# Performance work log

Measured on AMD Instinct MI355X. Metric: run time of the kernel, lower is better.

Reference implementation:

```python
import jax, jax.numpy as jnp
import numpy as np

N, K, P = 40000, 32, 15
C = 128            # output_feature_dim (kpconv in/out channels)
H_POS, D_POS = 64, 256
H_AGG, D_PROC = 256, 256
RADIUS = 1.0
KP_EXTENT = RADIUS / (P ** (1.0 / 3.0) - 1.0) * 1.5
SLOPE = 0.01       # nn.LeakyReLU default
EPS = 1e-5         # BatchNorm1d default eps


def _lin(key, din, dout):
    k1, k2 = jax.random.split(key)
    lim = 1.0 / np.sqrt(din)
    w = jax.random.uniform(k1, (din, dout), minval=-lim, maxval=lim, dtype=jnp.float32)
    b = jax.random.uniform(k2, (dout,), minval=-lim, maxval=lim, dtype=jnp.float32)
    return w, b


def _bn(x, g, b):
    # BatchNorm1d in training mode: biased batch statistics
    m = jnp.mean(x, axis=0)
    v = jnp.var(x, axis=0)
    return (x - m) * jax.lax.rsqrt(v + EPS) * g + b


def _lrelu(x):
    return jnp.where(x >= 0, x, SLOPE * x)


def setup_inputs() -> dict:
    key = jax.random.key(0)
    ks = jax.random.split(key, 16)
    inp = {}
    inp['points'] = jax.random.normal(ks[0], (N, 3), dtype=jnp.float32) * 10.0
    inp['covariances'] = jax.random.normal(ks[1], (N, 9), dtype=jnp.float32)
    inp['neighbors_index'] = jax.random.randint(ks[2], (N, K), 0, N)
    inp['pre_w'], inp['pre_b'] = _lin(ks[3], 9, C)
    inp['pre_bn_g'] = jnp.ones((C,), jnp.float32); inp['pre_bn_b'] = jnp.zeros((C,), jnp.float32)
    kp = jax.random.normal(ks[4], (P, 3), dtype=jnp.float32)
    kp = kp / jnp.linalg.norm(kp, axis=1, keepdims=True)
    inp['kernel_points'] = kp * jax.random.uniform(ks[5], (P, 1), dtype=jnp.float32) * RADIUS
    inp['kp_weights'] = jax.random.normal(ks[6], (P, C, C), dtype=jnp.float32) * (1.0 / np.sqrt(P * C))
    inp['pos_w1'], inp['pos_b1'] = _lin(ks[7], 3, H_POS)
    inp['pos_bn1_g'] = jnp.ones((H_POS,), jnp.float32); inp['pos_bn1_b'] = jnp.zeros((H_POS,), jnp.float32)
    inp['pos_w2'], inp['pos_b2'] = _lin(ks[8], H_POS, D_POS)
    inp['pos_bn2_g'] = jnp.ones((D_POS,), jnp.float32); inp['pos_bn2_b'] = jnp.zeros((D_POS,), jnp.float32)
    inp['agg_w1'], inp['agg_b1'] = _lin(ks[9], C, H_AGG)
    inp['agg_bn1_g'] = jnp.ones((H_AGG,), jnp.float32); inp['agg_bn1_b'] = jnp.zeros((H_AGG,), jnp.float32)
    inp['agg_w2'], inp['agg_b2'] = _lin(ks[10], H_AGG, D_PROC)
    inp['agg_bn2_g'] = jnp.ones((D_PROC,), jnp.float32); inp['agg_bn2_b'] = jnp.zeros((D_PROC,), jnp.float32)
    inp['keep_w1'], inp['keep_b1'] = _lin(ks[11], D_PROC, D_PROC // 4)
    inp['keep_bn_g'] = jnp.ones((D_PROC // 4,), jnp.float32); inp['keep_bn_b'] = jnp.zeros((D_PROC // 4,), jnp.float32)
    inp['keep_w2'], inp['keep_b2'] = _lin(ks[12], D_PROC // 4, 1)
    du = D_PROC + D_POS
    inp['uniq_w1'], inp['uniq_b1'] = _lin(ks[13], du, du // 4)
    inp['uniq_bn_g'] = jnp.ones((du // 4,), jnp.float32); inp['uniq_bn_b'] = jnp.zeros((du // 4,), jnp.float32)
    inp['uniq_w2'], inp['uniq_b2'] = _lin(ks[14], du // 4, 1)
    return inp


def reference(points, covariances, neighbors_index,
              pre_w, pre_b, pre_bn_g, pre_bn_b,
              kernel_points, kp_weights,
              pos_w1, pos_b1, pos_bn1_g, pos_bn1_b,
              pos_w2, pos_b2, pos_bn2_g, pos_bn2_b,
              agg_w1, agg_b1, agg_bn1_g, agg_bn1_b,
              agg_w2, agg_b2, agg_bn2_g, agg_bn2_b,
              keep_w1, keep_b1, keep_bn_g, keep_bn_b, keep_w2, keep_b2,
              uniq_w1, uniq_b1, uniq_bn_g, uniq_bn_b, uniq_w2, uniq_b2):
    # preactivation on 9-dim flattened covariances
    features = _lrelu(_bn(covariances @ pre_w + pre_b, pre_bn_g, pre_bn_b))  # [N, C]

    # ---- rigid KPConv (linear influence, sum aggregation, shadow point at index N) ----
    s_pad = jnp.concatenate([points, jnp.full((1, 3), 1e6, points.dtype)], axis=0)
    x_pad = jnp.concatenate([features, jnp.zeros((1, C), features.dtype)], axis=0)
    nb = s_pad[neighbors_index] - points[:, None, :]                          # [N, K, 3]
    # squared distances to kernel points without materializing [N,K,P,3]
    sq = (jnp.sum(nb * nb, -1)[:, :, None]
          + jnp.sum(kernel_points * kernel_points, -1)[None, None, :]
          - 2.0 * jnp.einsum('nkd,pd->nkp', nb, kernel_points))               # [N, K, P]
    infl = jnp.maximum(1.0 - jnp.sqrt(jnp.maximum(sq, 0.0)) / KP_EXTENT, 0.0)  # [N, K, P]
    nx = x_pad[neighbors_index]                                               # [N, K, C]
    weighted = jnp.einsum('nkp,nkc->npc', infl, nx)                           # [N, P, C]
    conv = jnp.einsum('npc,pcd->nd', weighted, kp_weights)                    # [N, C]
    # density normalization: count non-shadow neighbors
    nnum = jnp.maximum(jnp.sum(jnp.sum(nx, -1) > 0.0, axis=-1), 1)
    kpconv_feature = conv / nnum[:, None].astype(conv.dtype)

    # position embedding MLP
    pos = _lrelu(_bn(points @ pos_w1 + pos_b1, pos_bn1_g, pos_bn1_b))
    pos = _lrelu(_bn(pos @ pos_w2 + pos_b2, pos_bn2_g, pos_bn2_b))            # [N, 256]

    # feature aggregation MLP
    agg = _lrelu(_bn(kpconv_feature @ agg_w1 + agg_b1, agg_bn1_g, agg_bn1_b))
    agg = _lrelu(_bn(agg @ agg_w2 + agg_b2, agg_bn2_g, agg_bn2_b))            # [N, 256]

    # heads
    kh = _lrelu(_bn(agg @ keep_w1 + keep_b1, keep_bn_g, keep_bn_b))
    match_score = jax.nn.sigmoid((kh @ keep_w2 + keep_b2).ravel())
    u_in = jnp.concatenate([pos, agg], axis=1)                                # [N, 512]
    uh = _lrelu(_bn(u_in @ uniq_w1 + uniq_b1, uniq_bn_g, uniq_bn_b))
    unique_score = jax.nn.sigmoid((uh @ uniq_w2 + uniq_b2).ravel())
    return match_score, unique_score, neighbors_index
```

## Files before the change

### kernel.cpp

```cpp
#include <hip/hip_runtime.h>
#include <math.h>


#define NPTS 40000
#define KNB  32
#define PKP  15
#define SLOPE 0.01f
#define BNEPS 1e-5f
#define INV_N (1.0f/40000.0f)

typedef __attribute__((ext_vector_type(8))) short bf16x8;
typedef __attribute__((ext_vector_type(4))) float f32x4;

__device__ __forceinline__ float lrelu(float x){ return x >= 0.0f ? x : SLOPE*x; }
__device__ __forceinline__ unsigned short f2bf(float f){
  unsigned int b = __float_as_uint(f);
  b += 0x7fffu + ((b>>16)&1u);
  return (unsigned short)(b>>16);
}
__device__ __forceinline__ float bf2f(unsigned short u){
  return __uint_as_float(((unsigned int)u)<<16);
}

__global__ __launch_bounds__(256) void k_wprep_all(
    const float* __restrict__ kpw,  const float* __restrict__ pw2,
    const float* __restrict__ aw1,  const float* __restrict__ aw2,
    const float* __restrict__ kw1,  const float* __restrict__ uw1,
    unsigned short* __restrict__ wT){
  int i = blockIdx.x*256 + threadIdx.x;
  const float* src; int K, N, off, li;
  if      (i < 245760){ src=kpw; K=1920; N=128; off=0;      li=i; }
  else if (i < 262144){ src=pw2; K=64;   N=256; off=245760; li=i-245760; }
  else if (i < 294912){ src=aw1; K=128;  N=256; off=262144; li=i-262144; }
  else if (i < 360448){ src=aw2; K=256;  N=256; off=294912; li=i-294912; }
  else if (i < 376832){ src=kw1; K=256;  N=64;  off=360448; li=i-360448; }
  else                { src=uw1; K=512;  N=128; off=376832; li=i-376832; }
  int k = li / N, n = li - k*N;
  wT[(size_t)off + (size_t)n*K + k] = f2bf(src[li]);
}

__global__ __launch_bounds__(256) void k_pre(
    const float* __restrict__ cov, const float* __restrict__ w,
    const float* __restrict__ b, unsigned short* __restrict__ preact,
    float* __restrict__ stats){
  __shared__ float sW[9*128];
  __shared__ float sX[32*9];
  __shared__ float sSum[2][128], sSq[2][128];
  int tid = threadIdx.x;
  int row0 = blockIdx.x*32;
  for (int i = tid; i < 9*128; i += 256) sW[i] = w[i];
  for (int i = tid; i < 32*9;  i += 256) sX[i] = cov[row0*9 + i];
  __syncthreads();
  int c = tid & 127, h = tid >> 7;
  float bias = b[c];
  float ls = 0.0f, lq = 0.0f;
  for (int r = h*16; r < h*16+16; ++r){
    float acc = bias;
    #pragma unroll
    for (int i = 0; i < 9; ++i) acc += sX[r*9+i]*sW[i*128+c];
    preact[(size_t)(row0+r)*128 + c] = f2bf(acc);
    ls += acc; lq += acc*acc;
  }
  sSum[h][c] = ls; sSq[h][c] = lq;
  __syncthreads();
  if (h == 0){
    atomicAdd(&stats[c],     sSum[0][c]+sSum[1][c]);
    atomicAdd(&stats[128+c], sSq[0][c]+sSq[1][c]);
  }
}

__global__ __launch_bounds__(256) void k_prenorm(
    const unsigned short* __restrict__ preact, const float* __restrict__ stats,
    const float* __restrict__ g, const float* __restrict__ b,
    unsigned short* __restrict__ feat, float* __restrict__ fsum){
  int wid  = (int)((blockIdx.x*256 + threadIdx.x) >> 6);
  int lane = threadIdx.x & 63;
  if (wid >= NPTS) return;
  float su = stats[lane], sq = stats[128+lane];
  float mean = su*INV_N, var = sq*INV_N - mean*mean;
  float s0 = g[lane]*rsqrtf(var+BNEPS), h0 = b[lane]-mean*s0;
  su = stats[64+lane]; sq = stats[192+lane];
  mean = su*INV_N; var = sq*INV_N - mean*mean;
  float s1 = g[64+lane]*rsqrtf(var+BNEPS), h1 = b[64+lane]-mean*s1;
  size_t off = (size_t)wid*128;
  float f0 = lrelu(bf2f(preact[off+lane])*s0+h0);
  float f1 = lrelu(bf2f(preact[off+64+lane])*s1+h1);
  feat[off+lane]    = f2bf(f0);
  feat[off+64+lane] = f2bf(f1);
  float t = f0 + f1;
  #pragma unroll
  for (int o = 32; o; o >>= 1) t += __shfl_down(t, o, 64);
  if (lane == 0) fsum[wid] = t;
}

__global__ __launch_bounds__(256) void k_scan(
    const float* __restrict__ pts, const int* __restrict__ nbr,
    const float* __restrict__ kp, const float* __restrict__ fsum,
    float* __restrict__ invn, int* __restrict__ list,
    int* __restrict__ gcount, float ext2){
  __shared__ float sKP[45];
  if (threadIdx.x < 45) sKP[threadIdx.x] = kp[threadIdx.x];
  __syncthreads();
  int wv   = (blockIdx.x*256 + threadIdx.x) >> 6;
  int lane = threadIdx.x & 63;
  int half = lane >> 5;
  int kk   = lane & 31;
  int n    = wv*2 + half;
  float px = pts[n*3+0], py = pts[n*3+1], pz = pts[n*3+2];
  int j = nbr[(size_t)n*KNB + kk];
  float nx = pts[j*3+0] - px;
  float ny = pts[j*3+1] - py;
  float nz = pts[j*3+2] - pz;
  float fs = fsum[j];
  bool anyp = false;
  #pragma unroll
  for (int p = 0; p < PKP; ++p){
    float dx = nx - sKP[p*3+0], dy = ny - sKP[p*3+1], dz = nz - sKP[p*3+2];
    anyp |= (dx*dx + dy*dy + dz*dz < ext2);
  }
  unsigned long long act  = __ballot(anyp);
  unsigned long long good = __ballot(fs > 0.0f);
  unsigned int actH  = half ? (unsigned int)(act  >> 32) : (unsigned int)act;
  unsigned int goodH = half ? (unsigned int)(good >> 32) : (unsigned int)good;
  if (kk == 0){
    int cnt = __popc(goodH);
    invn[n] = 1.0f / (float)(cnt < 1 ? 1 : cnt);
    if (actH){
      int pos = atomicAdd(gcount, 1);
      list[pos] = n;
    }
  }
}

__global__ __launch_bounds__(256) void k_conv_act(
    const float* __restrict__ pts, const int* __restrict__ nbr,
    const float* __restrict__ kp, const unsigned short* __restrict__ feat,
    const unsigned short* __restrict__ kpwT, const float* __restrict__ invn,
    const int* __restrict__ list, const int* __restrict__ gcount,
    unsigned short* __restrict__ kpfc, float ext2, float inv_ext){
  __shared__ float sW[PKP*128];
  __shared__ float sInfl[KNB*16];
  __shared__ unsigned int sPairP[KNB];
  __shared__ float sKP[45];
  __shared__ float sOut[128];
  __shared__ unsigned int sPmask, sPact;
  int tid = threadIdx.x;
  if (tid < 45) sKP[tid] = kp[tid];
  int cnt = *gcount;
  for (int it = blockIdx.x; it < cnt; it += gridDim.x){
    int n = list[it];
    if (tid == 0){ sPmask = 0u; sPact = 0u; }
    for (int i = tid; i < PKP*128; i += 256) sW[i] = 0.0f;
    __syncthreads();
    if (tid < KNB){
      int j = nbr[(size_t)n*KNB + tid];
      float nx = pts[j*3+0] - pts[n*3+0];
      float ny = pts[j*3+1] - pts[n*3+1];
      float nz = pts[j*3+2] - pts[n*3+2];
      unsigned int pm = 0u;
      #pragma unroll
      for (int p = 0; p < PKP; ++p){
        float dx = nx - sKP[p*3+0], dy = ny - sKP[p*3+1], dz = nz - sKP[p*3+2];
        float d2 = dx*dx + dy*dy + dz*dz;
        float infl = 0.0f;
        if (d2 < ext2){ infl = 1.0f - sqrtf(d2)*inv_ext; pm |= (1u << p); }
        sInfl[tid*16 + p] = infl;
      }
      sPairP[tid] = pm;
      if (pm){
        atomicOr(&sPact, 1u << tid);
        atomicOr(&sPmask, pm);
      }
    }
    __syncthreads();
    if (tid < 128){
      int c = tid;
      unsigned int m = sPact;
      while (m){
        int k = __ffs(m) - 1; m &= m - 1;
        int j = nbr[(size_t)n*KNB + k];
        float f = bf2f(feat[(size_t)j*128 + c]);
        unsigned int pp = sPairP[k];
        while (pp){
          int p = __ffs(pp) - 1; pp &= pp - 1;
          sW[p*128 + c] += sInfl[k*16 + p] * f;
        }
      }
    }
    __syncthreads();
    int d = tid & 127, h = tid >> 7;
    float acc = 0.0f;
    unsigned int pm = sPmask;
    while (pm){
      int p = __ffs(pm) - 1; pm &= pm - 1;
      const unsigned short* wp = kpwT + (size_t)d*1920 + p*128 + h*64;
      const float* wsrc = &sW[p*128 + h*64];
      #pragma unroll
      for (int c8 = 0; c8 < 8; ++c8){
        uint4 v = *(const uint4*)(wp + c8*8);
        unsigned int e[4] = {v.x, v.y, v.z, v.w};
        #pragma unroll
        for (int q = 0; q < 4; ++q){
          acc += wsrc[c8*8 + 2*q]     * bf2f((unsigned short)(e[q] & 0xffff));
          acc += wsrc[c8*8 + 2*q + 1] * bf2f((unsigned short)(e[q] >> 16));
        }
      }
    }
    if (h == 0) sOut[d] = acc;
    __syncthreads();
    if (h == 1) kpfc[(size_t)it*128 + d] = f2bf((sOut[d] + acc) * invn[n]);
    __syncthreads();
  }
}

__global__ __launch_bounds__(256) void k_rowgemm(
    const unsigned short* __restrict__ X, int xCompact,
    const float* __restrict__ st, const float* __restrict__ g,
    const float* __restrict__ bb, int K, int norm,
    const unsigned short* __restrict__ Wt, const float* __restrict__ bias,
    int NOUT, unsigned short* __restrict__ Y, int yCompact,
    float* __restrict__ statsOut,
    const int* __restrict__ list, const int* __restrict__ gcount){
  __shared__ float xs[256];
  __shared__ float sSc[256], sSh[256];
  int tid = threadIdx.x;
  if (norm && tid < K){
    float s = st[tid], q = st[K+tid];
    float mean = s*INV_N, var = q*INV_N - mean*mean;
    float sc = g[tid]*rsqrtf(var+BNEPS);
    sSc[tid] = sc; sSh[tid] = bb[tid] - mean*sc;
  }
  __syncthreads();
  int cnt = *gcount;
  float rs = 0.0f, rq = 0.0f;
  for (int it = blockIdx.x; it < cnt; it += gridDim.x){
    int n = list[it];
    int xi = xCompact ? it : n;
    if (tid < K){
      float xv = bf2f(X[(size_t)xi*K + tid]);
      if (norm) xv = lrelu(xv*sSc[tid] + sSh[tid]);
      xs[tid] = xv;
    }
    __syncthreads();
    if (tid < NOUT){
      float acc = bias[tid];
      const unsigned short* wp = Wt + (size_t)tid*K;
      for (int k8 = 0; k8 < K; k8 += 8){
        uint4 v = *(const uint4*)(wp + k8);
        unsigned int e[4] = {v.x, v.y, v.z, v.w};
        #pragma unroll
        for (int q = 0; q < 4; ++q){
          acc += xs[k8+2*q]   * bf2f((unsigned short)(e[q] & 0xffff));
          acc += xs[k8+2*q+1] * bf2f((unsigned short)(e[q] >> 16));
        }
      }
      int yi = yCompact ? it : n;
      Y[(size_t)yi*NOUT + tid] = f2bf(acc);
      rs += acc; rq += acc*acc;
    }
    __syncthreads();
  }
  if (tid < NOUT && rs != 0.0f){
    atomicAdd(&statsOut[tid],      rs);
    atomicAdd(&statsOut[NOUT+tid], rq);
  }
}

__global__ __launch_bounds__(256) void k_const(
    const float* __restrict__ vin, float* __restrict__ statsX, int K,
    const float* __restrict__ g, const float* __restrict__ bb,
    const unsigned short* __restrict__ Wt, const float* __restrict__ bias,
    int NOUT, float* __restrict__ vout, unsigned int* __restrict__ voutU,
    const int* __restrict__ gcount){
  __shared__ float sX[256];
  __shared__ float sV[256];
  int tid = threadIdx.x;
  float fN = (float)(NPTS - *gcount);
  if (tid < K){
    float s = vin[tid];
    statsX[tid]   += fN*s;
    statsX[K+tid] += fN*s*s;
  }
  __syncthreads();
  if (NOUT > 0){
    if (tid < K){
      float s = statsX[tid], q = statsX[K+tid];
      float mean = s*INV_N, var = q*INV_N - mean*mean;
      float sc = g[tid]*rsqrtf(var+BNEPS);
      sX[tid] = lrelu(vin[tid]*sc + bb[tid] - mean*sc);
    }
    __syncthreads();
    if (tid < NOUT){
      float acc = bias[tid];
      const unsigned short* wp = Wt + (size_t)tid*K;
      for (int k8 = 0; k8 < K; k8 += 8){
        uint4 v = *(const uint4*)(wp + k8);
        unsigned int e[4] = {v.x, v.y, v.z, v.w};
        #pragma unroll
        for (int q = 0; q < 4; ++q){
          acc += sX[k8+2*q]   * bf2f((unsigned short)(e[q] & 0xffff));
          acc += sX[k8+2*q+1] * bf2f((unsigned short)(e[q] >> 16));
        }
      }
      vout[tid] = acc; sV[tid] = acc;
    }
    __syncthreads();
    if (tid < NOUT/2)
      voutU[tid] = (unsigned int)f2bf(sV[2*tid]) |
                   ((unsigned int)f2bf(sV[2*tid+1]) << 16);
  }
}

__global__ __launch_bounds__(256) void k_fill(
    unsigned int* __restrict__ Y, const unsigned int* __restrict__ vU,
    int shift, int total){
  int i = blockIdx.x*256 + threadIdx.x;
  int stride = gridDim.x*256;
  unsigned int msk = (1u << shift) - 1u;
  for (; i < total; i += stride) Y[i] = vU[i & msk];
}

template<int NCF>
__global__ __launch_bounds__(256) void k_gemmw(
    const unsigned short* __restrict__ X0, const float* __restrict__ st0,
    const float* __restrict__ g0, const float* __restrict__ b0,
    int K0, int norm0,
    const unsigned short* __restrict__ X1, const float* __restrict__ st1,
    const float* __restrict__ g1, const float* __restrict__ b1, int K1,
    const unsigned short* __restrict__ Wt, const float* __restrict__ bias,
    unsigned short* __restrict__ Y, float* __restrict__ statsOut){
  const int NOUT = NCF*16;
  __shared__ unsigned short sA[64*64];
  __shared__ unsigned short sB[NOUT*64];
  __shared__ float sSc[64], sSh[64];
  __shared__ float sSum[NOUT], sSq[NOUT];
  int tid = threadIdx.x;
  int row0 = blockIdx.x*64;
  int w = tid >> 6, l = tid & 63;
  int KT = K0 + K1;
  if (tid < NOUT){ sSum[tid] = 0.0f; sSq[tid] = 0.0f; }
  f32x4 acc[NCF] = {};
  for (int kc = 0; kc < KT; kc += 64){
    bool sel1 = (kc >= K0);
    const unsigned short* Xp = sel1 ? X1 : X0;
    int Ks = sel1 ? K1 : K0;
    int cb = sel1 ? kc - K0 : kc;
    int nf = sel1 ? 1 : norm0;
    if (tid < 64 && nf){
      const float* st = sel1 ? st1 : st0;
      const float* gg = sel1 ? g1 : g0;
      const float* bb = sel1 ? b1 : b0;
      int ch = cb + tid;
      float s = st[ch], q = st[Ks+ch];
      float mean = s*INV_N, var = q*INV_N - mean*mean;
      float sc = gg[ch]*rsqrtf(var+BNEPS);
      sSc[tid] = sc; sSh[tid] = bb[ch] - mean*sc;
    }
    __syncthreads();
    #pragma unroll
    for (int p = 0; p < 2; ++p){
      int r = (tid >> 3) + p*32;
      int k0 = (tid & 7)*8;
      uint4 v = *(const uint4*)(Xp + (size_t)(row0+r)*Ks + cb + k0);
      if (nf){
        unsigned short e[8] = {(unsigned short)(v.x&0xffff),(unsigned short)(v.x>>16),
                               (unsigned short)(v.y&0xffff),(unsigned short)(v.y>>16),
                               (unsigned short)(v.z&0xffff),(unsigned short)(v.z>>16),
                               (unsigned short)(v.w&0xffff),(unsigned short)(v.w>>16)};
        unsigned short o[8];
        #pragma unroll
        for (int j = 0; j < 8; ++j)
          o[j] = f2bf(lrelu(bf2f(e[j])*sSc[k0+j] + sSh[k0+j]));
        v.x = (uint)o[0] | ((uint)o[1]<<16);
        v.y = (uint)o[2] | ((uint)o[3]<<16);
        v.z = (uint)o[4] | ((uint)o[5]<<16);
        v.w = (uint)o[6] | ((uint)o[7]<<16);
      }
      int byteA = (r*128 + k0*2) ^ ((r&7)<<4);
      *(uint4*)((char*)sA + byteA) = v;
    }
    #pragma unroll
    for (int ps = 0; ps < NCF/2; ++ps){
      int idx = ps*256 + tid;
      int r = idx >> 3, s = idx & 7;
      uint4 vb = *(const uint4*)(Wt + (size_t)r*KT + kc + s*8);
      int byteB = (r*128 + s*16) ^ ((r&7)<<4);
      *(uint4*)((char*)sB + byteB) = vb;
    }
    __syncthreads();
    int rowA = w*16 + (l & 15);
    #pragma unroll
    for (int m = 0; m < 2; ++m){
      int ka = m*32 + (l >> 4)*8;
      int byteA = (rowA*128 + ka*2) ^ ((rowA&7)<<4);
      bf16x8 af = *(const bf16x8*)((const char*)sA + byteA);
      #pragma unroll
      for (int cf = 0; cf < NCF; ++cf){
        int colB = cf*16 + (l & 15);
        int byteB = (colB*128 + ka*2) ^ ((colB&7)<<4);
        bf16x8 bfr = *(const bf16x8*)((const char*)sB + byteB);
        acc[cf] = __builtin_amdgcn_mfma_f32_16x16x32_bf16(af, bfr, acc[cf], 0, 0, 0);
      }
    }
    __syncthreads();
  }
  float cs[NCF], cq[NCF];
  #pragma unroll
  for (int cf = 0; cf < NCF; ++cf){
    int col = cf*16 + (l & 15);
    float bj = bias[col];
    cs[cf] = 0.0f; cq[cf] = 0.0f;
    #pragma unroll
    for (int r = 0; r < 4; ++r){
      int grow = row0 + w*16 + (l >> 4)*4 + r;
      float v = acc[cf][r] + bj;
      Y[(size_t)grow*NOUT + col] = f2bf(v);
      cs[cf] += v; cq[cf] += v*v;
    }
  }
  #pragma unroll
  for (int cf = 0; cf < NCF; ++cf){
    atomicAdd(&sSum[cf*16 + (l&15)], cs[cf]);
    atomicAdd(&sSq[cf*16 + (l&15)],  cq[cf]);
  }
  __syncthreads();
  if (tid < NOUT){
    atomicAdd(&statsOut[tid],      sSum[tid]);
    atomicAdd(&statsOut[NOUT+tid], sSq[tid]);
  }
}

__global__ __launch_bounds__(256) void k_pos1(
    const float* __restrict__ pts, const float* __restrict__ w,
    const float* __restrict__ b, unsigned short* __restrict__ p1,
    float* __restrict__ stats){
  __shared__ float sSum[4][64], sSq[4][64];
  int tid = threadIdx.x;
  int c = tid & 63, grp = tid >> 6;
  int row0 = blockIdx.x*32;
  float w0 = w[c], w1 = w[64+c], w2 = w[128+c], bb = b[c];
  float ls = 0.0f, lq = 0.0f;
  for (int r = row0 + grp*8; r < row0 + grp*8 + 8; ++r){
    float x0 = pts[r*3+0], x1 = pts[r*3+1], x2 = pts[r*3+2];
    float y = bb + x0*w0 + x1*w1 + x2*w2;
    p1[(size_t)r*64 + c] = f2bf(y);
    ls += y; lq += y*y;
  }
  sSum[grp][c] = ls; sSq[grp][c] = lq;
  __syncthreads();
  if (grp == 0){
    atomicAdd(&stats[c],    sSum[0][c]+sSum[1][c]+sSum[2][c]+sSum[3][c]);
    atomicAdd(&stats[64+c], sSq[0][c]+sSq[1][c]+sSq[2][c]+sSq[3][c]);
  }
}

__global__ __launch_bounds__(256) void k_head(
    const unsigned short* __restrict__ H, const float* __restrict__ stats,
    const float* __restrict__ g, const float* __restrict__ b,
    const float* __restrict__ w2, const float* __restrict__ b2,
    float* __restrict__ out, int Cdim){
  int wid  = (int)((blockIdx.x*256 + threadIdx.x) >> 6);
  int lane = threadIdx.x & 63;
  if (wid >= NPTS) return;
  float acc = 0.0f;
  for (int c = lane; c < Cdim; c += 64){
    float su = stats[c], sq = stats[Cdim+c];
    float mean = su*INV_N, var = sq*INV_N - mean*mean;
    float sc = g[c]*rsqrtf(var+BNEPS), sh = b[c]-mean*sc;
    float h = lrelu(bf2f(H[(size_t)wid*Cdim + c])*sc + sh);
    acc += h * w2[c];
  }
  #pragma unroll
  for (int o = 32; o; o >>= 1) acc += __shfl_down(acc, o, 64);
  if (lane == 0){
    float x = acc + b2[0];
    out[wid] = 1.0f/(1.0f + expf(-x));
  }
}

__global__ __launch_bounds__(256) void k_idx(
    const int* __restrict__ nbr, float* __restrict__ o){
  int i = blockIdx.x*256 + threadIdx.x;
  int4 v = ((const int4*)nbr)[i];
  ((float4*)o)[i] = make_float4((float)v.x,(float)v.y,(float)v.z,(float)v.w);
}

extern "C" void kernel_launch(void* const* d_in, const int* in_sizes, int n_in,
                              void* d_out, int out_size, void* d_ws, size_t ws_size,
                              hipStream_t stream) {
  const float* pts    = (const float*)d_in[0];
  const float* cov    = (const float*)d_in[1];
  const int*   nbr    = (const int*)  d_in[2];
  const float* pre_w  = (const float*)d_in[3];
  const float* pre_b  = (const float*)d_in[4];
  const float* pre_g  = (const float*)d_in[5];
  const float* pre_bb = (const float*)d_in[6];
  const float* kp     = (const float*)d_in[7];
  const float* kpw    = (const float*)d_in[8];
  const float* pos_w1 = (const float*)d_in[9];
  const float* pos_b1 = (const float*)d_in[10];
  const float* pos_g1 = (const float*)d_in[11];
  const float* pos_bb1= (const float*)d_in[12];
  const float* pos_w2 = (const float*)d_in[13];
  const float* pos_b2 = (const float*)d_in[14];
  const float* pos_g2 = (const float*)d_in[15];
  const float* pos_bb2= (const float*)d_in[16];
  const float* agg_w1 = (const float*)d_in[17];
  const float* agg_b1 = (const float*)d_in[18];
  const float* agg_g1 = (const float*)d_in[19];
  const float* agg_bb1= (const float*)d_in[20];
  const float* agg_w2 = (const float*)d_in[21];
  const float* agg_b2 = (const float*)d_in[22];
  const float* agg_g2 = (const float*)d_in[23];
  const float* agg_bb2= (const float*)d_in[24];
  const float* keep_w1= (const float*)d_in[25];
  const float* keep_b1= (const float*)d_in[26];
  const float* keep_g = (const float*)d_in[27];
  const float* keep_bb= (const float*)d_in[28];
  const float* keep_w2= (const float*)d_in[29];
  const float* keep_b2= (const float*)d_in[30];
  const float* uniq_w1= (const float*)d_in[31];
  const float* uniq_b1= (const float*)d_in[32];
  const float* uniq_g = (const float*)d_in[33];
  const float* uniq_bb= (const float*)d_in[34];
  const float* uniq_w2= (const float*)d_in[35];
  const float* uniq_b2= (const float*)d_in[36];

  float* out = (float*)d_out;

  char* wsb = (char*)d_ws;
  size_t off = 0;
  float* stats = (float*)(wsb + off); off += 4096*4;
  int*   gcount = (int*)(stats + 2304);
  float* v2  = stats + 2560;
  unsigned int* v2u = (unsigned int*)(stats + 2816);
  float* v3  = stats + 2944;
  unsigned int* v3u = (unsigned int*)(stats + 3008);
  unsigned short* wT = (unsigned short*)(wsb + off); off += (size_t)442368*2;
  unsigned short* kpwT   = wT;
  unsigned short* posw2T = wT + 245760;
  unsigned short* aggw1T = wT + 262144;
  unsigned short* aggw2T = wT + 294912;
  unsigned short* keepw1T= wT + 360448;
  unsigned short* uniqw1T= wT + 376832;
  float* fsum  = (float*)(wsb + off); off += (size_t)NPTS*4;
  float* invn  = (float*)(wsb + off); off += (size_t)NPTS*4;
  int*   list  = (int*)  (wsb + off); off += (size_t)NPTS*4;
  unsigned short* feat = (unsigned short*)(wsb + off); off += (size_t)NPTS*128*2;
  unsigned short* kpfc = (unsigned short*)(wsb + off); off += (size_t)NPTS*128*2;
  unsigned short* a1c  = (unsigned short*)(wsb + off); off += (size_t)NPTS*256*2;
  unsigned short* a2   = (unsigned short*)(wsb + off); off += (size_t)NPTS*256*2;
  unsigned short* k1   = (unsigned short*)(wsb + off); off += (size_t)NPTS*64*2;
  unsigned short* preact = a2;
  unsigned short* p1 = feat;
  unsigned short* p2 = a1c;
  unsigned short* u1 = kpfc;

  const double kpe = 1.0 / (cbrt(15.0) - 1.0) * 1.5;
  const float inv_ext = (float)(1.0 / kpe);
  const float ext2 = (float)(kpe * kpe);

  hipMemsetAsync(stats, 0, 2308*sizeof(float), stream);

  k_wprep_all<<<1728, 256, 0, stream>>>(kpw, pos_w2, agg_w1, agg_w2,
                                        keep_w1, uniq_w1, wT);

  k_pre<<<1250, 256, 0, stream>>>(cov, pre_w, pre_b, preact, stats + 0);
  k_prenorm<<<10000, 256, 0, stream>>>(preact, stats + 0, pre_g, pre_bb, feat, fsum);

  k_scan<<<5000, 256, 0, stream>>>(pts, nbr, kp, fsum, invn, list, gcount, ext2);
  k_conv_act<<<1024, 256, 0, stream>>>(pts, nbr, kp, feat, kpwT, invn,
                                       list, gcount, kpfc, ext2, inv_ext);

  k_pos1<<<1250, 256, 0, stream>>>(pts, pos_w1, pos_b1, p1, stats + 256);

  k_rowgemm<<<256, 256, 0, stream>>>(
      kpfc, 1, nullptr, nullptr, nullptr, 128, 0,
      aggw1T, agg_b1, 256, a1c, 1, stats + 896, list, gcount);
  k_const<<<1, 256, 0, stream>>>(
      agg_b1, stats + 896, 256, agg_g1, agg_bb1,
      aggw2T, agg_b2, 256, v2, v2u, gcount);
  k_fill<<<2048, 256, 0, stream>>>((unsigned int*)a2, v2u, 7, NPTS*128);
  k_rowgemm<<<256, 256, 0, stream>>>(
      a1c, 1, stats + 896, agg_g1, agg_bb1, 256, 1,
      aggw2T, agg_b2, 256, a2, 0, stats + 1408, list, gcount);
  k_const<<<1, 256, 0, stream>>>(
      v2, stats + 1408, 256, agg_g2, agg_bb2,
      keepw1T, keep_b1, 64, v3, v3u, gcount);
  k_fill<<<2048, 256, 0, stream>>>((unsigned int*)k1, v3u, 5, NPTS*32);
  k_rowgemm<<<256, 256, 0, stream>>>(
      a2, 0, stats + 1408, agg_g2, agg_bb2, 256, 1,
      keepw1T, keep_b1, 64, k1, 0, stats + 1920, list, gcount);
  k_const<<<1, 256, 0, stream>>>(
      v3, stats + 1920, 64, nullptr, nullptr,
      nullptr, nullptr, 0, nullptr, nullptr, gcount);

  k_gemmw<16><<<625, 256, 0, stream>>>(
      p1, stats + 256, pos_g1, pos_bb1, 64, 1,
      nullptr, nullptr, nullptr, nullptr, 0,
      posw2T, pos_b2, p2, stats + 384);

  k_head<<<10000, 256, 0, stream>>>(k1, stats + 1920, keep_g, keep_bb,
                                    keep_w2, keep_b2, out, 64);

  k_gemmw<8><<<625, 256, 0, stream>>>(
      p2, stats + 384, pos_g2, pos_bb2, 256, 1,
      a2, stats + 1408, agg_g2, agg_bb2, 256,
      uniqw1T, uniq_b1, u1, stats + 2048);
  k_head<<<10000, 256, 0, stream>>>(u1, stats + 2048, uniq_g, uniq_bb,
                                    uniq_w2, uniq_b2, out + NPTS, 128);

  k_idx<<<1250, 256, 0, stream>>>(nbr, out + 2*NPTS);
}
```

Measured before the change: 314.7 us.

## Compute BN stats analytically from moments and exploit sparse active rows end-to-end

Replaces the pre-layer GEMM-then-normalize passes with input moment accumulation, so BatchNorm statistics for the pre and first position layers are derived in closed form. The feature and position MLP stages are fused into single kernels. The aggregation chain now stays compact over active rows: a constant row value is propagated for inactive points instead of filling full buffers. The uniqueness GEMM is split into a dense position part with an effective bias plus a sparse delta for active rows. This removes large intermediate writes and fill kernels, at the cost of variance computed from raw moments, which may lose precision.

```diff
diff --git a/kernel.cpp b/kernel.cpp
--- a/kernel.cpp
+++ b/kernel.cpp
@@ -21,6 +21,7 @@
 __device__ __forceinline__ float bf2f(unsigned short u){
   return __uint_as_float(((unsigned int)u)<<16);
 }
+
 
 __global__ __launch_bounds__(256) void k_wprep_all(
     const float* __restrict__ kpw,  const float* __restrict__ pw2,
@@ -39,58 +40,104 @@
   wT[(size_t)off + (size_t)n*K + k] = f2bf(src[li]);
 }
 
-__global__ __launch_bounds__(256) void k_pre(
-    const float* __restrict__ cov, const float* __restrict__ w,
-    const float* __restrict__ b, unsigned short* __restrict__ preact,
+__global__ __launch_bounds__(256) void k_moments(
+    const float* __restrict__ cov, const float* __restrict__ pts,
+    float* __restrict__ mom){
+  int tid = threadIdx.x;
+  int lane = tid & 63;
+  int wv = (blockIdx.x*256 + tid) >> 6;
+  int nw = gridDim.x*4;
+  int kind = -1, ia = 0, ib = 0;
+  if (lane < 9){ kind = 0; ia = lane; }
+  else if (lane < 54){ int t = lane-9; int i = 0; while (t >= 9-i){ t -= 9-i; ++i; } kind = 1; ia = i; ib = i+t; }
+  else if (lane < 57){ kind = 2; ia = lane-54; }
+  else if (lane < 63){ int t = lane-57; int i = 0; while (t >= 3-i){ t -= 3-i; ++i; } kind = 3; ia = i; ib = i+t; }
+  float part = 0.0f;
+  for (int n = wv; n < NPTS; n += nw){
+    float v = 0.0f;
+    if (kind == 0) v = cov[n*9+ia];
+    else if (kind == 1) v = cov[n*9+ia]*cov[n*9+ib];
+    else if (kind == 2) v = pts[n*3+ia];
+    else if (kind == 3) v = pts[n*3+ia]*pts[n*3+ib];
+    part += v;
+  }
+  if (kind >= 0) atomicAdd(&mom[lane], part);
+}
+
+__global__ __launch_bounds__(256) void k_bnsetup(
+    const float* __restrict__ preW, const float* __restrict__ preB,
+    const float* __restrict__ preG, const float* __restrict__ preBB,
+    const float* __restrict__ posW1, const float* __restrict__ posB1,
+    const float* __restrict__ posG1, const float* __restrict__ posBB1,
     float* __restrict__ stats){
-  __shared__ float sW[9*128];
-  __shared__ float sX[32*9];
-  __shared__ float sSum[2][128], sSq[2][128];
-  int tid = threadIdx.x;
-  int row0 = blockIdx.x*32;
-  for (int i = tid; i < 9*128; i += 256) sW[i] = w[i];
-  for (int i = tid; i < 32*9;  i += 256) sX[i] = cov[row0*9 + i];
-  __syncthreads();
-  int c = tid & 127, h = tid >> 7;
-  float bias = b[c];
-  float ls = 0.0f, lq = 0.0f;
-  for (int r = h*16; r < h*16+16; ++r){
-    float acc = bias;
-    #pragma unroll
-    for (int i = 0; i < 9; ++i) acc += sX[r*9+i]*sW[i*128+c];
-    preact[(size_t)(row0+r)*128 + c] = f2bf(acc);
-    ls += acc; lq += acc*acc;
-  }
-  sSum[h][c] = ls; sSq[h][c] = lq;
-  __syncthreads();
-  if (h == 0){
-    atomicAdd(&stats[c],     sSum[0][c]+sSum[1][c]);
-    atomicAdd(&stats[128+c], sSq[0][c]+sSq[1][c]);
-  }
-}
-
-__global__ __launch_bounds__(256) void k_prenorm(
-    const unsigned short* __restrict__ preact, const float* __restrict__ stats,
-    const float* __restrict__ g, const float* __restrict__ b,
-    unsigned short* __restrict__ feat, float* __restrict__ fsum){
-  int wid  = (int)((blockIdx.x*256 + threadIdx.x) >> 6);
-  int lane = threadIdx.x & 63;
-  if (wid >= NPTS) return;
-  float su = stats[lane], sq = stats[128+lane];
-  float mean = su*INV_N, var = sq*INV_N - mean*mean;
-  float s0 = g[lane]*rsqrtf(var+BNEPS), h0 = b[lane]-mean*s0;
-  su = stats[64+lane]; sq = stats[192+lane];
-  mean = su*INV_N; var = sq*INV_N - mean*mean;
-  float s1 = g[64+lane]*rsqrtf(var+BNEPS), h1 = b[64+lane]-mean*s1;
-  size_t off = (size_t)wid*128;
-  float f0 = lrelu(bf2f(preact[off+lane])*s0+h0);
-  float f1 = lrelu(bf2f(preact[off+64+lane])*s1+h1);
-  feat[off+lane]    = f2bf(f0);
-  feat[off+64+lane] = f2bf(f1);
-  float t = f0 + f1;
-  #pragma unroll
-  for (int o = 32; o; o >>= 1) t += __shfl_down(t, o, 64);
-  if (lane == 0) fsum[wid] = t;
+  int tid = threadIdx.x;
+  const float* mom = stats + 2320;
+  if (tid < 128){
+    int c = tid;
+    float wv[9];
+    #pragma unroll
+    for (int i = 0; i < 9; ++i) wv[i] = preW[i*128+c];
+    float b = preB[c];
+    float mw = 0.0f;
+    #pragma unroll
+    for (int i = 0; i < 9; ++i) mw += wv[i]*mom[i];
+    mw *= INV_N;
+    float quad = 0.0f;
+    for (int i = 0; i < 9; ++i)
+      for (int j = 0; j < 9; ++j){
+        int ii = i < j ? i : j, jj = i < j ? j : i;
+        quad += wv[i]*wv[j]*mom[9 + ii*9 - (ii*(ii-1))/2 + (jj-ii)];
+      }
+    quad *= INV_N;
+    float mean = mw + b;
+    float var = quad + 2.0f*b*mw + b*b - mean*mean;
+    float sc = preG[c]*rsqrtf(var+BNEPS);
+    stats[c]     = sc;
+    stats[128+c] = preBB[c] - mean*sc + sc*b;
+  } else if (tid < 192){
+    int c = tid - 128;
+    float w0 = posW1[c], w1 = posW1[64+c], w2 = posW1[128+c];
+    float b = posB1[c];
+    const float* pm = mom + 54;
+    const float* pM = mom + 57;
+    float mw = (w0*pm[0] + w1*pm[1] + w2*pm[2])*INV_N;
+    float quad = (w0*w0*pM[0] + w1*w1*pM[3] + w2*w2*pM[5]
+               + 2.0f*(w0*w1*pM[1] + w0*w2*pM[2] + w1*w2*pM[4]))*INV_N;
+    float mean = mw + b;
+    float var = quad + 2.0f*b*mw + b*b - mean*mean;
+    float sc = posG1[c]*rsqrtf(var+BNEPS);
+    stats[256+c] = sc;
+    stats[320+c] = posBB1[c] - mean*sc + sc*b;
+  }
+}
+
+__global__ __launch_bounds__(256) void k_feat(
+    const float* __restrict__ cov, const float* __restrict__ preW,
+    const float* __restrict__ stats, unsigned short* __restrict__ feat,
+    float* __restrict__ fsum){
+  __shared__ float sW[1152];
+  __shared__ float sRed[4];
+  int tid = threadIdx.x;
+  for (int i = tid; i < 1152; i += 256) sW[i] = preW[i];
+  int c = tid & 127, g = tid >> 7;
+  float sc = stats[c], sh = stats[128+c];
+  __syncthreads();
+  for (int base = blockIdx.x*2; base < NPTS; base += gridDim.x*2){
+    int row = base + g;
+    float pre = 0.0f;
+    #pragma unroll
+    for (int i = 0; i < 9; ++i) pre += cov[row*9+i]*sW[i*128+c];
+    float f = lrelu(sc*pre + sh);
+    feat[(size_t)row*128 + c] = f2bf(f);
+    float t = f;
+    #pragma unroll
+    for (int o = 32; o; o >>= 1) t += __shfl_down(t, o, 64);
+    if ((tid & 63) == 0) sRed[tid>>6] = t;
+    __syncthreads();
+    if (tid == 0)   fsum[base]   = sRed[0] + sRed[1];
+    if (tid == 128) fsum[base+1] = sRed[2] + sRed[3];
+    __syncthreads();
+  }
 }
 
 __global__ __launch_bounds__(256) void k_scan(
@@ -213,13 +260,71 @@
   }
 }
 
+__global__ __launch_bounds__(256) void k_pos(
+    const float* __restrict__ pts, const float* __restrict__ posW1,
+    const float* __restrict__ stats, const unsigned short* __restrict__ w2T,
+    const float* __restrict__ b2, unsigned short* __restrict__ p2,
+    float* __restrict__ st384){
+  __shared__ unsigned short sW[16384];
+  __shared__ float sX[4][64];
+  __shared__ unsigned short sP2[1024];
+  int tid = threadIdx.x;
+  #pragma unroll
+  for (int ps = 0; ps < 8; ++ps){
+    int idx = ps*256 + tid;
+    int r = idx >> 3, s = idx & 7;
+    uint4 v = *(const uint4*)(w2T + (size_t)r*64 + s*8);
+    *(uint4*)((char*)sW + ((r*128 + s*16) ^ ((r&7)<<4))) = v;
+  }
+  int k = tid & 63, g = tid >> 6;
+  float w0 = posW1[k], w1 = posW1[64+k], w2 = posW1[128+k];
+  float sc1 = stats[256+k], sh1 = stats[320+k];
+  int c = tid;
+  float b2c = b2[c];
+  float cs = 0.0f, cq = 0.0f;
+  __syncthreads();
+  for (int base = blockIdx.x*4; base < NPTS; base += gridDim.x*4){
+    int row = base + g;
+    float x0 = pts[row*3+0], x1 = pts[row*3+1], x2 = pts[row*3+2];
+    sX[g][k] = lrelu(sc1*(x0*w0 + x1*w1 + x2*w2) + sh1);
+    __syncthreads();
+    float acc[4] = {b2c, b2c, b2c, b2c};
+    #pragma unroll
+    for (int k8 = 0; k8 < 64; k8 += 8){
+      uint4 v = *(const uint4*)((const char*)sW + ((c*128 + k8*2) ^ ((c&7)<<4)));
+      unsigned int e[4] = {v.x, v.y, v.z, v.w};
+      #pragma unroll
+      for (int q = 0; q < 4; ++q){
+        float wlo = bf2f((unsigned short)(e[q] & 0xffff));
+        float whi = bf2f((unsigned short)(e[q] >> 16));
+        #pragma unroll
+        for (int r = 0; r < 4; ++r)
+          acc[r] += sX[r][k8+2*q]*wlo + sX[r][k8+2*q+1]*whi;
+      }
+    }
+    #pragma unroll
+    for (int r = 0; r < 4; ++r){
+      cs += acc[r]; cq += acc[r]*acc[r];
+      sP2[r*256 + c] = f2bf(acc[r]);
+    }
+    __syncthreads();
+    if (tid < 128){
+      int r = tid >> 5, c8 = tid & 31;
+      uint4 v = *(const uint4*)(sP2 + r*256 + c8*8);
+      *(uint4*)(p2 + (size_t)(base+r)*256 + c8*8) = v;
+    }
+    __syncthreads();
+  }
+  atomicAdd(&st384[c], cs);
+  atomicAdd(&st384[256+c], cq);
+}
+
 __global__ __launch_bounds__(256) void k_rowgemm(
-    const unsigned short* __restrict__ X, int xCompact,
+    const unsigned short* __restrict__ X,
     const float* __restrict__ st, const float* __restrict__ g,
     const float* __restrict__ bb, int K, int norm,
     const unsigned short* __restrict__ Wt, const float* __restrict__ bias,
-    int NOUT, unsigned short* __restrict__ Y, int yCompact,
-    float* __restrict__ statsOut,
+    int NOUT, unsigned short* __restrict__ Y, float* __restrict__ statsOut,
     const int* __restrict__ list, const int* __restrict__ gcount){
   __shared__ float xs[256];
   __shared__ float sSc[256], sSh[256];
@@ -234,10 +339,8 @@
   int cnt = *gcount;
   float rs = 0.0f, rq = 0.0f;
   for (int it = blockIdx.x; it < cnt; it += gridDim.x){
-    int n = list[it];
-    int xi = xCompact ? it : n;
     if (tid < K){
-      float xv = bf2f(X[(size_t)xi*K + tid]);
+      float xv = bf2f(X[(size_t)it*K + tid]);
       if (norm) xv = lrelu(xv*sSc[tid] + sSh[tid]);
       xs[tid] = xv;
     }
@@ -254,8 +357,7 @@
           acc += xs[k8+2*q+1] * bf2f((unsigned short)(e[q] >> 16));
         }
       }
-      int yi = yCompact ? it : n;
-      Y[(size_t)yi*NOUT + tid] = f2bf(acc);
+      Y[(size_t)it*NOUT + tid] = f2bf(acc);
       rs += acc; rq += acc*acc;
     }
     __syncthreads();
@@ -266,34 +368,256 @@
   }
 }
 
-__global__ __launch_bounds__(256) void k_const(
-    const float* __restrict__ vin, float* __restrict__ statsX, int K,
+__global__ __launch_bounds__(256) void k_const1(
+    const float* __restrict__ b1, const float* __restrict__ g1,
+    const float* __restrict__ bb1, const unsigned short* __restrict__ aggw2T,
+    const float* __restrict__ b2, float* __restrict__ st896,
+    float* __restrict__ v2, const int* __restrict__ gcount){
+  __shared__ float sX[256];
+  int tid = threadIdx.x;
+  float fN = (float)(NPTS - *gcount);
+  float s = b1[tid];
+  st896[tid]     += fN*s;
+  st896[256+tid] += fN*s*s;
+  float su = st896[tid], sq = st896[256+tid];
+  float mean = su*INV_N, var = sq*INV_N - mean*mean;
+  float sc = g1[tid]*rsqrtf(var+BNEPS);
+  sX[tid] = lrelu(s*sc + bb1[tid] - mean*sc);
+  __syncthreads();
+  float acc = b2[tid];
+  const unsigned short* wp = aggw2T + (size_t)tid*256;
+  for (int k8 = 0; k8 < 256; k8 += 8){
+    uint4 v = *(const uint4*)(wp + k8);
+    unsigned int e[4] = {v.x, v.y, v.z, v.w};
+    #pragma unroll
+    for (int q = 0; q < 4; ++q){
+      acc += sX[k8+2*q]   * bf2f((unsigned short)(e[q] & 0xffff));
+      acc += sX[k8+2*q+1] * bf2f((unsigned short)(e[q] >> 16));
+    }
+  }
+  v2[tid] = acc;
+}
+
+__global__ __launch_bounds__(256) void k_const2(
+    const float* __restrict__ v2, const float* __restrict__ g2,
+    const float* __restrict__ bb2, const unsigned short* __restrict__ keepw1T,
+    const float* __restrict__ kb1, const unsigned short* __restrict__ uw1T,
+    const float* __restrict__ ub1, float* __restrict__ st1408,
+    float* __restrict__ v3, float* __restrict__ ub_eff,
+    const int* __restrict__ gcount){
+  __shared__ float sX[256];
+  int tid = threadIdx.x;
+  float fN = (float)(NPTS - *gcount);
+  float s = v2[tid];
+  st1408[tid]     += fN*s;
+  st1408[256+tid] += fN*s*s;
+  float su = st1408[tid], sq = st1408[256+tid];
+  float mean = su*INV_N, var = sq*INV_N - mean*mean;
+  float sc = g2[tid]*rsqrtf(var+BNEPS);
+  sX[tid] = lrelu(s*sc + bb2[tid] - mean*sc);
+  __syncthreads();
+  if (tid < 64){
+    float acc = kb1[tid];
+    const unsigned short* wp = keepw1T + (size_t)tid*256;
+    for (int k8 = 0; k8 < 256; k8 += 8){
+      uint4 v = *(const uint4*)(wp + k8);
+      unsigned int e[4] = {v.x, v.y, v.z, v.w};
+      #pragma unroll
+      for (int q = 0; q < 4; ++q){
+        acc += sX[k8+2*q]   * bf2f((unsigned short)(e[q] & 0xffff));
+        acc += sX[k8+2*q+1] * bf2f((unsigned short)(e[q] >> 16));
+      }
+    }
+    v3[tid] = acc;
+  } else if (tid < 192){
+    int c = tid - 64;
+    float acc = ub1[c];
+    const unsigned short* wp = uw1T + (size_t)c*512 + 256;
+    for (int k8 = 0; k8 < 256; k8 += 8){
+      uint4 v = *(const uint4*)(wp + k8);
+      unsigned int e[4] = {v.x, v.y, v.z, v.w};
+      #pragma unroll
+      for (int q = 0; q < 4; ++q){
+        acc += sX[k8+2*q]   * bf2f((unsigned short)(e[q] & 0xffff));
+        acc += sX[k8+2*q+1] * bf2f((unsigned short)(e[q] >> 16));
+      }
+    }
+    ub_eff[c] = acc;
+  }
+}
+
+__global__ __launch_bounds__(64) void k_const3(
+    const float* __restrict__ v3, const float* __restrict__ g3,
+    const float* __restrict__ bb3, const float* __restrict__ kw2,
+    const float* __restrict__ kb2, float* __restrict__ st1920,
+    float* __restrict__ s3out, const int* __restrict__ gcount){
+  int tid = threadIdx.x;
+  float fN = (float)(NPTS - *gcount);
+  float s = v3[tid];
+  st1920[tid]    += fN*s;
+  st1920[64+tid] += fN*s*s;
+  float su = st1920[tid], sq = st1920[64+tid];
+  float mean = su*INV_N, var = sq*INV_N - mean*mean;
+  float sc = g3[tid]*rsqrtf(var+BNEPS);
+  float h = lrelu(s*sc + bb3[tid] - mean*sc) * kw2[tid];
+  #pragma unroll
+  for (int o = 32; o; o >>= 1) h += __shfl_down(h, o, 64);
+  if (tid == 0) s3out[0] = 1.0f/(1.0f + expf(-(h + kb2[0])));
+}
+
+__global__ __launch_bounds__(256) void k_out(
+    const int* __restrict__ nbr, const float* __restrict__ s3p,
+    float* __restrict__ out){
+  int i = blockIdx.x*256 + threadIdx.x;
+  if (i < NPTS) out[i] = s3p[0];
+  int4 v = ((const int4*)nbr)[i];
+  ((float4*)(out + 2*NPTS))[i] =
+      make_float4((float)v.x,(float)v.y,(float)v.z,(float)v.w);
+}
+
+__global__ __launch_bounds__(256) void k_keepact(
+    const unsigned short* __restrict__ k1c, const float* __restrict__ st1920,
+    const float* __restrict__ g3, const float* __restrict__ b3,
+    const float* __restrict__ w2, const float* __restrict__ b2,
+    float* __restrict__ out, const int* __restrict__ list,
+    const int* __restrict__ gcount){
+  int tid = threadIdx.x;
+  int lane = tid & 63;
+  int wv = (blockIdx.x*256 + tid) >> 6;
+  int nw = gridDim.x*4;
+  float su = st1920[lane], sq = st1920[64+lane];
+  float mean = su*INV_N, var = sq*INV_N - mean*mean;
+  float sc = g3[lane]*rsqrtf(var+BNEPS);
+  float sh = b3[lane] - mean*sc;
+  float w2v = w2[lane];
+  int cnt = *gcount;
+  for (int it = wv; it < cnt; it += nw){
+    float h = lrelu(bf2f(k1c[(size_t)it*64 + lane])*sc + sh) * w2v;
+    #pragma unroll
+    for (int o = 32; o; o >>= 1) h += __shfl_down(h, o, 64);
+    if (lane == 0) out[list[it]] = 1.0f/(1.0f + expf(-(h + b2[0])));
+  }
+}
+
+__global__ __launch_bounds__(256) void k_ugemm(
+    const unsigned short* __restrict__ X, const float* __restrict__ st,
     const float* __restrict__ g, const float* __restrict__ bb,
     const unsigned short* __restrict__ Wt, const float* __restrict__ bias,
-    int NOUT, float* __restrict__ vout, unsigned int* __restrict__ voutU,
+    unsigned short* __restrict__ Y, float* __restrict__ statsOut){
+  __shared__ unsigned short sA[4096];
+  __shared__ unsigned short sB[8704];
+  __shared__ float sSc[64], sSh[64];
+  __shared__ float sSum[128], sSq[128];
+  int tid = threadIdx.x;
+  int row0 = blockIdx.x*64;
+  int w = tid >> 6, l = tid & 63;
+  if (tid < 128){ sSum[tid] = 0.0f; sSq[tid] = 0.0f; }
+  f32x4 acc[8] = {};
+  for (int kc = 0; kc < 256; kc += 64){
+    if (tid < 64){
+      int ch = kc + tid;
+      float s = st[ch], q = st[256+ch];
+      float mean = s*INV_N, var = q*INV_N - mean*mean;
+      float sc = g[ch]*rsqrtf(var+BNEPS);
+      sSc[tid] = sc; sSh[tid] = bb[ch] - mean*sc;
+    }
+    __syncthreads();
+    #pragma unroll
+    for (int p = 0; p < 2; ++p){
+      int r = (tid >> 3) + p*32;
+      int k0 = (tid & 7)*8;
+      uint4 v = *(const uint4*)(X + (size_t)(row0+r)*256 + kc + k0);
+      unsigned short e[8] = {(unsigned short)(v.x&0xffff),(unsigned short)(v.x>>16),
+                             (unsigned short)(v.y&0xffff),(unsigned short)(v.y>>16),
+                             (unsigned short)(v.z&0xffff),(unsigned short)(v.z>>16),
+                             (unsigned short)(v.w&0xffff),(unsigned short)(v.w>>16)};
+      unsigned short o[8];
+      #pragma unroll
+      for (int j = 0; j < 8; ++j)
+        o[j] = f2bf(lrelu(bf2f(e[j])*sSc[k0+j] + sSh[k0+j]));
+      v.x = (uint)o[0] | ((uint)o[1]<<16);
+      v.y = (uint)o[2] | ((uint)o[3]<<16);
+      v.z = (uint)o[4] | ((uint)o[5]<<16);
+      v.w = (uint)o[6] | ((uint)o[7]<<16);
+      *(uint4*)((char*)sA + ((r*128 + k0*2) ^ ((r&7)<<4))) = v;
+    }
+    #pragma unroll
+    for (int ps = 0; ps < 4; ++ps){
+      int idx = ps*256 + tid;
+      int r = idx >> 3, s = idx & 7;
+      uint4 vb = *(const uint4*)(Wt + (size_t)r*512 + kc + s*8);
+      *(uint4*)((char*)sB + ((r*128 + s*16) ^ ((r&7)<<4))) = vb;
+    }
+    __syncthreads();
+    int rowA = w*16 + (l & 15);
+    #pragma unroll
+    for (int m = 0; m < 2; ++m){
+      int ka = m*32 + (l >> 4)*8;
+      bf16x8 af = *(const bf16x8*)((const char*)sA + ((rowA*128 + ka*2) ^ ((rowA&7)<<4)));
+      #pragma unroll
+      for (int cf = 0; cf < 8; ++cf){
+        int colB = cf*16 + (l & 15);
+        bf16x8 bfr = *(const bf16x8*)((const char*)sB + ((colB*128 + ka*2) ^ ((colB&7)<<4)));
+        acc[cf] = __builtin_amdgcn_mfma_f32_16x16x32_bf16(af, bfr, acc[cf], 0, 0, 0);
+      }
+    }
+    __syncthreads();
+  }
+  #pragma unroll
+  for (int cf = 0; cf < 8; ++cf){
+    int col = cf*16 + (l & 15);
+    float bj = bias[col];
+    float cs = 0.0f, cq = 0.0f;
+    #pragma unroll
+    for (int r = 0; r < 4; ++r){
+      int rr = w*16 + (l >> 4)*4 + r;
+      float v = acc[cf][r] + bj;
+      sB[rr*136 + col] = f2bf(v);
+      cs += v; cq += v*v;
+    }
+    atomicAdd(&sSum[col], cs);
+    atomicAdd(&sSq[col],  cq);
+  }
+  __syncthreads();
+  #pragma unroll
+  for (int ps = 0; ps < 4; ++ps){
+    int idx = ps*256 + tid;
+    int r = idx >> 4, c8 = idx & 15;
+    uint4 v = *(const uint4*)((const char*)sB + r*272 + c8*16);
+    *(uint4*)(Y + (size_t)(row0+r)*128 + c8*8) = v;
+  }
+  if (tid < 128){
+    atomicAdd(&statsOut[tid],     sSum[tid]);
+    atomicAdd(&statsOut[128+tid], sSq[tid]);
+  }
+}
+
+__global__ __launch_bounds__(256) void k_udelta(
+    const unsigned short* __restrict__ a2c, const float* __restrict__ st1408,
+    const float* __restrict__ g2, const float* __restrict__ bb2,
+    const unsigned short* __restrict__ uw1T, const float* __restrict__ ub1,
+    const float* __restrict__ ub_eff, unsigned short* __restrict__ u1,
+    float* __restrict__ st2048, const int* __restrict__ list,
     const int* __restrict__ gcount){
   __shared__ float sX[256];
-  __shared__ float sV[256];
-  int tid = threadIdx.x;
-  float fN = (float)(NPTS - *gcount);
-  if (tid < K){
-    float s = vin[tid];
-    statsX[tid]   += fN*s;
-    statsX[K+tid] += fN*s*s;
-  }
-  __syncthreads();
-  if (NOUT > 0){
-    if (tid < K){
-      float s = statsX[tid], q = statsX[K+tid];
-      float mean = s*INV_N, var = q*INV_N - mean*mean;
-      float sc = g[tid]*rsqrtf(var+BNEPS);
-      sX[tid] = lrelu(vin[tid]*sc + bb[tid] - mean*sc);
-    }
-    __syncthreads();
-    if (tid < NOUT){
-      float acc = bias[tid];
-      const unsigned short* wp = Wt + (size_t)tid*K;
-      for (int k8 = 0; k8 < K; k8 += 8){
+  __shared__ float sSc[256], sSh[256];
+  int tid = threadIdx.x;
+  {
+    float su = st1408[tid], sq = st1408[256+tid];
+    float mean = su*INV_N, var = sq*INV_N - mean*mean;
+    float sc = g2[tid]*rsqrtf(var+BNEPS);
+    sSc[tid] = sc; sSh[tid] = bb2[tid] - mean*sc;
+  }
+  __syncthreads();
+  int cnt = *gcount;
+  for (int it = blockIdx.x; it < cnt; it += gridDim.x){
+    int n = list[it];
+    sX[tid] = lrelu(bf2f(a2c[(size_t)it*256 + tid])*sSc[tid] + sSh[tid]);
+    __syncthreads();
+    if (tid < 128){
+      float acc = ub1[tid] - ub_eff[tid];
+      const unsigned short* wp = uw1T + (size_t)tid*512 + 256;
+      for (int k8 = 0; k8 < 256; k8 += 8){
         uint4 v = *(const uint4*)(wp + k8);
         unsigned int e[4] = {v.x, v.y, v.z, v.w};
         #pragma unroll
@@ -302,187 +626,42 @@
           acc += sX[k8+2*q+1] * bf2f((unsigned short)(e[q] >> 16));
         }
       }
-      vout[tid] = acc; sV[tid] = acc;
-    }
-    __syncthreads();
-    if (tid < NOUT/2)
-      voutU[tid] = (unsigned int)f2bf(sV[2*tid]) |
-                   ((unsigned int)f2bf(sV[2*tid+1]) << 16);
-  }
-}
-
-__global__ __launch_bounds__(256) void k_fill(
-    unsigned int* __restrict__ Y, const unsigned int* __restrict__ vU,
-    int shift, int total){
-  int i = blockIdx.x*256 + threadIdx.x;
-  int stride = gridDim.x*256;
-  unsigned int msk = (1u << shift) - 1u;
-  for (; i < total; i += stride) Y[i] = vU[i & msk];
-}
-
-template<int NCF>
-__global__ __launch_bounds__(256) void k_gemmw(
-    const unsigned short* __restrict__ X0, const float* __restrict__ st0,
-    const float* __restrict__ g0, const float* __restrict__ b0,
-    int K0, int norm0,
-    const unsigned short* __restrict__ X1, const float* __restrict__ st1,
-    const float* __restrict__ g1, const float* __restrict__ b1, int K1,
-    const unsigned short* __restrict__ Wt, const float* __restrict__ bias,
-    unsigned short* __restrict__ Y, float* __restrict__ statsOut){
-  const int NOUT = NCF*16;
-  __shared__ unsigned short sA[64*64];
-  __shared__ unsigned short sB[NOUT*64];
-  __shared__ float sSc[64], sSh[64];
-  __shared__ float sSum[NOUT], sSq[NOUT];
-  int tid = threadIdx.x;
-  int row0 = blockIdx.x*64;
-  int w = tid >> 6, l = tid & 63;
-  int KT = K0 + K1;
-  if (tid < NOUT){ sSum[tid] = 0.0f; sSq[tid] = 0.0f; }
-  f32x4 acc[NCF] = {};
-  for (int kc = 0; kc < KT; kc += 64){
-    bool sel1 = (kc >= K0);
-    const unsigned short* Xp = sel1 ? X1 : X0;
-    int Ks = sel1 ? K1 : K0;
-    int cb = sel1 ? kc - K0 : kc;
-    int nf = sel1 ? 1 : norm0;
-    if (tid < 64 && nf){
-      const float* st = sel1 ? st1 : st0;
-      const float* gg = sel1 ? g1 : g0;
-      const float* bb = sel1 ? b1 : b0;
-      int ch = cb + tid;
-      float s = st[ch], q = st[Ks+ch];
-      float mean = s*INV_N, var = q*INV_N - mean*mean;
-      float sc = gg[ch]*rsqrtf(var+BNEPS);
-      sSc[tid] = sc; sSh[tid] = bb[ch] - mean*sc;
-    }
-    __syncthreads();
-    #pragma unroll
-    for (int p = 0; p < 2; ++p){
-      int r = (tid >> 3) + p*32;
-      int k0 = (tid & 7)*8;
-      uint4 v = *(const uint4*)(Xp + (size_t)(row0+r)*Ks + cb + k0);
-      if (nf){
-        unsigned short e[8] = {(unsigned short)(v.x&0xffff),(unsigned short)(v.x>>16),
-                               (unsigned short)(v.y&0xffff),(unsigned short)(v.y>>16),
-                               (unsigned short)(v.z&0xffff),(unsigned short)(v.z>>16),
-                               (unsigned short)(v.w&0xffff),(unsigned short)(v.w>>16)};
-        unsigned short o[8];
-        #pragma unroll
-        for (int j = 0; j < 8; ++j)
-          o[j] = f2bf(lrelu(bf2f(e[j])*sSc[k0+j] + sSh[k0+j]));
-        v.x = (uint)o[0] | ((uint)o[1]<<16);
-        v.y = (uint)o[2] | ((uint)o[3]<<16);
-        v.z = (uint)o[4] | ((uint)o[5]<<16);
-        v.w = (uint)o[6] | ((uint)o[7]<<16);
-      }
-      int byteA = (r*128 + k0*2) ^ ((r&7)<<4);
-      *(uint4*)((char*)sA + byteA) = v;
-    }
-    #pragma unroll
-    for (int ps = 0; ps < NCF/2; ++ps){
-      int idx = ps*256 + tid;
-      int r = idx >> 3, s = idx & 7;
-      uint4 vb = *(const uint4*)(Wt + (size_t)r*KT + kc + s*8);
-      int byteB = (r*128 + s*16) ^ ((r&7)<<4);
-      *(uint4*)((char*)sB + byteB) = vb;
-    }
-    __syncthreads();
-    int rowA = w*16 + (l & 15);
-    #pragma unroll
-    for (int m = 0; m < 2; ++m){
-      int ka = m*32 + (l >> 4)*8;
-      int byteA = (rowA*128 + ka*2) ^ ((rowA&7)<<4);
-      bf16x8 af = *(const bf16x8*)((const char*)sA + byteA);
-      #pragma unroll
-      for (int cf = 0; cf < NCF; ++cf){
-        int colB = cf*16 + (l & 15);
-        int byteB = (colB*128 + ka*2) ^ ((colB&7)<<4);
-        bf16x8 bfr = *(const bf16x8*)((const char*)sB + byteB);
-        acc[cf] = __builtin_amdgcn_mfma_f32_16x16x32_bf16(af, bfr, acc[cf], 0, 0, 0);
-      }
-    }
-    __syncthreads();
-  }
-  float cs[NCF], cq[NCF];
-  #pragma unroll
-  for (int cf = 0; cf < NCF; ++cf){
-    int col = cf*16 + (l & 15);
-    float bj = bias[col];
-    cs[cf] = 0.0f; cq[cf] = 0.0f;
-    #pragma unroll
-    for (int r = 0; r < 4; ++r){
-      int grow = row0 + w*16 + (l >> 4)*4 + r;
-      float v = acc[cf][r] + bj;
-      Y[(size_t)grow*NOUT + col] = f2bf(v);
-      cs[cf] += v; cq[cf] += v*v;
-    }
-  }
-  #pragma unroll
-  for (int cf = 0; cf < NCF; ++cf){
-    atomicAdd(&sSum[cf*16 + (l&15)], cs[cf]);
-    atomicAdd(&sSq[cf*16 + (l&15)],  cq[cf]);
-  }
-  __syncthreads();
-  if (tid < NOUT){
-    atomicAdd(&statsOut[tid],      sSum[tid]);
-    atomicAdd(&statsOut[NOUT+tid], sSq[tid]);
-  }
-}
-
-__global__ __launch_bounds__(256) void k_pos1(
-    const float* __restrict__ pts, const float* __restrict__ w,
-    const float* __restrict__ b, unsigned short* __restrict__ p1,
-    float* __restrict__ stats){
-  __shared__ float sSum[4][64], sSq[4][64];
-  int tid = threadIdx.x;
-  int c = tid & 63, grp = tid >> 6;
-  int row0 = blockIdx.x*32;
-  float w0 = w[c], w1 = w[64+c], w2 = w[128+c], bb = b[c];
-  float ls = 0.0f, lq = 0.0f;
-  for (int r = row0 + grp*8; r < row0 + grp*8 + 8; ++r){
-    float x0 = pts[r*3+0], x1 = pts[r*3+1], x2 = pts[r*3+2];
-    float y = bb + x0*w0 + x1*w1 + x2*w2;
-    p1[(size_t)r*64 + c] = f2bf(y);
-    ls += y; lq += y*y;
-  }
-  sSum[grp][c] = ls; sSq[grp][c] = lq;
-  __syncthreads();
-  if (grp == 0){
-    atomicAdd(&stats[c],    sSum[0][c]+sSum[1][c]+sSum[2][c]+sSum[3][c]);
-    atomicAdd(&stats[64+c], sSq[0][c]+sSq[1][c]+sSq[2][c]+sSq[3][c]);
-  }
-}
-
-__global__ __launch_bounds__(256) void k_head(
-    const unsigned short* __restrict__ H, const float* __restrict__ stats,
+      float old = bf2f(u1[(size_t)n*128 + tid]);
+      float neu = old + acc;
+      u1[(size_t)n*128 + tid] = f2bf(neu);
+      atomicAdd(&st2048[tid],     neu - old);
+      atomicAdd(&st2048[128+tid], neu*neu - old*old);
+    }
+    __syncthreads();
+  }
+}
+
+__global__ __launch_bounds__(256) void k_uhead(
+    const unsigned short* __restrict__ u1, const float* __restrict__ st2048,
     const float* __restrict__ g, const float* __restrict__ b,
     const float* __restrict__ w2, const float* __restrict__ b2,
-    float* __restrict__ out, int Cdim){
-  int wid  = (int)((blockIdx.x*256 + threadIdx.x) >> 6);
-  int lane = threadIdx.x & 63;
-  if (wid >= NPTS) return;
-  float acc = 0.0f;
-  for (int c = lane; c < Cdim; c += 64){
-    float su = stats[c], sq = stats[Cdim+c];
+    float* __restrict__ out){
+  __shared__ float sSc[128], sSh[128], sW2[128];
+  int tid = threadIdx.x;
+  if (tid < 128){
+    float su = st2048[tid], sq = st2048[128+tid];
     float mean = su*INV_N, var = sq*INV_N - mean*mean;
-    float sc = g[c]*rsqrtf(var+BNEPS), sh = b[c]-mean*sc;
-    float h = lrelu(bf2f(H[(size_t)wid*Cdim + c])*sc + sh);
-    acc += h * w2[c];
-  }
-  #pragma unroll
-  for (int o = 32; o; o >>= 1) acc += __shfl_down(acc, o, 64);
-  if (lane == 0){
-    float x = acc + b2[0];
-    out[wid] = 1.0f/(1.0f + expf(-x));
-  }
-}
-
-__global__ __launch_bounds__(256) void k_idx(
-    const int* __restrict__ nbr, float* __restrict__ o){
-  int i = blockIdx.x*256 + threadIdx.x;
-  int4 v = ((const int4*)nbr)[i];
-  ((float4*)o)[i] = make_float4((float)v.x,(float)v.y,(float)v.z,(float)v.w);
+    float sc = g[tid]*rsqrtf(var+BNEPS);
+    sSc[tid] = sc; sSh[tid] = b[tid] - mean*sc;
+    sW2[tid] = w2[tid];
+  }
+  __syncthreads();
+  int lane = tid & 63, w = tid >> 6;
+  int nw = gridDim.x*4;
+  for (int n = blockIdx.x*4 + w; n < NPTS; n += nw){
+    unsigned int v = *(const unsigned int*)(u1 + (size_t)n*128 + lane*2);
+    int c0 = lane*2, c1 = c0 + 1;
+    float h = lrelu(bf2f((unsigned short)(v & 0xffff))*sSc[c0] + sSh[c0])*sW2[c0]
+            + lrelu(bf2f((unsigned short)(v >> 16))*sSc[c1] + sSh[c1])*sW2[c1];
+    #pragma unroll
+    for (int o = 32; o; o >>= 1) h += __shfl_down(h, o, 64);
+    if (lane == 0) out[n] = 1.0f/(1.0f + expf(-(h + b2[0])));
+  }
 }
 
 extern "C" void kernel_launch(void* const* d_in, const int* in_sizes, int n_in,
@@ -532,10 +711,11 @@
   size_t off = 0;
   float* stats = (float*)(wsb + off); off += 4096*4;
   int*   gcount = (int*)(stats + 2304);
-  float* v2  = stats + 2560;
-  unsigned int* v2u = (unsigned int*)(stats + 2816);
-  float* v3  = stats + 2944;
-  unsigned int* v3u = (unsigned int*)(stats + 3008);
+  float* s3     = stats + 2305;
+  float* mom    = stats + 2320;
+  float* v2     = stats + 2384;
+  float* v3     = stats + 2640;
+  float* ub_eff = stats + 2704;
   unsigned short* wT = (unsigned short*)(wsb + off); off += (size_t)442368*2;
   unsigned short* kpwT   = wT;
   unsigned short* posw2T = wT + 245760;
@@ -543,72 +723,61 @@
   unsigned short* aggw2T = wT + 294912;
   unsigned short* keepw1T= wT + 360448;
   unsigned short* uniqw1T= wT + 376832;
-  float* fsum  = (float*)(wsb + off); off += (size_t)NPTS*4;
-  float* invn  = (float*)(wsb + off); off += (size_t)NPTS*4;
-  int*   list  = (int*)  (wsb + off); off += (size_t)NPTS*4;
+  float* fsum = (float*)(wsb + off); off += (size_t)NPTS*4;
+  float* invn = (float*)(wsb + off); off += (size_t)NPTS*4;
+  int*   list = (int*)  (wsb + off); off += (size_t)NPTS*4;
   unsigned short* feat = (unsigned short*)(wsb + off); off += (size_t)NPTS*128*2;
   unsigned short* kpfc = (unsigned short*)(wsb + off); off += (size_t)NPTS*128*2;
   unsigned short* a1c  = (unsigned short*)(wsb + off); off += (size_t)NPTS*256*2;
-  unsigned short* a2   = (unsigned short*)(wsb + off); off += (size_t)NPTS*256*2;
-  unsigned short* k1   = (unsigned short*)(wsb + off); off += (size_t)NPTS*64*2;
-  unsigned short* preact = a2;
-  unsigned short* p1 = feat;
-  unsigned short* p2 = a1c;
-  unsigned short* u1 = kpfc;
+  unsigned short* a2c  = (unsigned short*)(wsb + off); off += (size_t)NPTS*256*2;
+  unsigned short* k1c  = (unsigned short*)(wsb + off); off += (size_t)NPTS*64*2;
+  unsigned short* p2   = (unsigned short*)(wsb + off); off += (size_t)NPTS*256*2;
+  unsigned short* u1   = (unsigned short*)(wsb + off); off += (size_t)NPTS*128*2;
 
   const double kpe = 1.0 / (cbrt(15.0) - 1.0) * 1.5;
   const float inv_ext = (float)(1.0 / kpe);
   const float ext2 = (float)(kpe * kpe);
 
-  hipMemsetAsync(stats, 0, 2308*sizeof(float), stream);
+  hipMemsetAsync(stats, 0, 2384*sizeof(float), stream);
 
   k_wprep_all<<<1728, 256, 0, stream>>>(kpw, pos_w2, agg_w1, agg_w2,
                                         keep_w1, uniq_w1, wT);
-
-  k_pre<<<1250, 256, 0, stream>>>(cov, pre_w, pre_b, preact, stats + 0);
-  k_prenorm<<<10000, 256, 0, stream>>>(preact, stats + 0, pre_g, pre_bb, feat, fsum);
-
+  k_moments<<<128, 256, 0, stream>>>(cov, pts, mom);
+  k_bnsetup<<<1, 256, 0, stream>>>(pre_w, pre_b, pre_g, pre_bb,
+                                   pos_w1, pos_b1, pos_g1, pos_bb1, stats);
+  k_feat<<<1024, 256, 0, stream>>>(cov, pre_w, stats, feat, fsum);
   k_scan<<<5000, 256, 0, stream>>>(pts, nbr, kp, fsum, invn, list, gcount, ext2);
   k_conv_act<<<1024, 256, 0, stream>>>(pts, nbr, kp, feat, kpwT, invn,
                                        list, gcount, kpfc, ext2, inv_ext);
-
-  k_pos1<<<1250, 256, 0, stream>>>(pts, pos_w1, pos_b1, p1, stats + 256);
-
-  k_rowgemm<<<256, 256, 0, stream>>>(
-      kpfc, 1, nullptr, nullptr, nullptr, 128, 0,
-      aggw1T, agg_b1, 256, a1c, 1, stats + 896, list, gcount);
-  k_const<<<1, 256, 0, stream>>>(
-      agg_b1, stats + 896, 256, agg_g1, agg_bb1,
-      aggw2T, agg_b2, 256, v2, v2u, gcount);
-  k_fill<<<2048, 256, 0, stream>>>((unsigned int*)a2, v2u, 7, NPTS*128);
-  k_rowgemm<<<256, 256, 0, stream>>>(
-      a1c, 1, stats + 896, agg_g1, agg_bb1, 256, 1,
-      aggw2T, agg_b2, 256, a2, 0, stats + 1408, list, gcount);
-  k_const<<<1, 256, 0, stream>>>(
-      v2, stats + 1408, 256, agg_g2, agg_bb2,
-      keepw1T, keep_b1, 64, v3, v3u, gcount);
-  k_fill<<<2048, 256, 0, stream>>>((unsigned int*)k1, v3u, 5, NPTS*32);
-  k_rowgemm<<<256, 256, 0, stream>>>(
-      a2, 0, stats + 1408, agg_g2, agg_bb2, 256, 1,
-      keepw1T, keep_b1, 64, k1, 0, stats + 1920, list, gcount);
-  k_const<<<1, 256, 0, stream>>>(
-      v3, stats + 1920, 64, nullptr, nullptr,
-      nullptr, nullptr, 0, nullptr, nullptr, gcount);
-
-  k_gemmw<16><<<625, 256, 0, stream>>>(
-      p1, stats + 256, pos_g1, pos_bb1, 64, 1,
-      nullptr, nullptr, nullptr, nullptr, 0,
-      posw2T, pos_b2, p2, stats + 384);
-
-  k_head<<<10000, 256, 0, stream>>>(k1, stats + 1920, keep_g, keep_bb,
-                                    keep_w2, keep_b2, out, 64);
-
-  k_gemmw<8><<<625, 256, 0, stream>>>(
-      p2, stats + 384, pos_g2, pos_bb2, 256, 1,
-      a2, stats + 1408, agg_g2, agg_bb2, 256,
-      uniqw1T, uniq_b1, u1, stats + 2048);
-  k_head<<<10000, 256, 0, stream>>>(u1, stats + 2048, uniq_g, uniq_bb,
-                                    uniq_w2, uniq_b2, out + NPTS, 128);
-
-  k_idx<<<1250, 256, 0, stream>>>(nbr, out + 2*NPTS);
-}
+  k_pos<<<1024, 256, 0, stream>>>(pts, pos_w1, stats, posw2T, pos_b2,
+                                  p2, stats + 384);
+
+  k_rowgemm<<<256, 256, 0, stream>>>(kpfc, nullptr, nullptr, nullptr, 128, 0,
+                                     aggw1T, agg_b1, 256, a1c, stats + 896,
+                                     list, gcount);
+  k_const1<<<1, 256, 0, stream>>>(agg_b1, agg_g1, agg_bb1, aggw2T, agg_b2,
+                                  stats + 896, v2, gcount);
+  k_rowgemm<<<256, 256, 0, stream>>>(a1c, stats + 896, agg_g1, agg_bb1, 256, 1,
+                                     aggw2T, agg_b2, 256, a2c, stats + 1408,
+                                     list, gcount);
+  k_const2<<<1, 256, 0, stream>>>(v2, agg_g2, agg_bb2, keepw1T, keep_b1,
+                                  uniqw1T, uniq_b1, stats + 1408, v3, ub_eff,
+                                  gcount);
+  k_rowgemm<<<256, 256, 0, stream>>>(a2c, stats + 1408, agg_g2, agg_bb2, 256, 1,
+                                     keepw1T, keep_b1, 64, k1c, stats + 1920,
+                                     list, gcount);
+  k_const3<<<1, 64, 0, stream>>>(v3, keep_g, keep_bb, keep_w2, keep_b2,
+                                 stats + 1920, s3, gcount);
+
+  k_out<<<1250, 256, 0, stream>>>(nbr, s3, out);
+  k_keepact<<<32, 256, 0, stream>>>(k1c, stats + 1920, keep_g, keep_bb,
+                                    keep_w2, keep_b2, out, list, gcount);
+
+  k_ugemm<<<625, 256, 0, stream>>>(p2, stats + 384, pos_g2, pos_bb2,
+                                   uniqw1T, ub_eff, u1, stats + 2048);
+  k_udelta<<<128, 256, 0, stream>>>(a2c, stats + 1408, agg_g2, agg_bb2,
+                                    uniqw1T, uniq_b1, ub_eff, u1, stats + 2048,
+                                    list, gcount);
+  k_uhead<<<2500, 256, 0, stream>>>(u1, stats + 2048, uniq_g, uniq_bb,
+                                    uniq_w2, uniq_b2, out + NPTS);
+}
```

Result: slower. 356.9 us (+13.4%).
